# Kernel tuning notes

Measured on AMD Instinct MI355X. Metric: run time of the kernel, lower is better.

## Reference

```python
import jax, jax.numpy as jnp
import numpy as np

SP = 4      # sp_size (number of simulated sequence-parallel ranks)
NH = 16     # num_attention_heads
HD = 64     # head_dim
HS = 1024   # hidden_size
B = 1       # batch
S = 8192    # global sequence length (SP chunks of 2048)


def setup_inputs() -> dict:
    key = jax.random.key(0)
    ks = jax.random.split(key, 9)
    w_scale = 1.0 / np.sqrt(HS)
    def w(k):
        # xavier-ish init, stored as [in, out] so y = x @ W + b
        return jax.random.uniform(k, (HS, HS), jnp.float32, -w_scale, w_scale)
    return {
        'hidden_states': jax.random.normal(ks[0], (B, S, HS), jnp.float32),
        'Wq': w(ks[1]), 'bq': jnp.zeros((HS,), jnp.float32),
        'Wk': w(ks[2]), 'bk': jnp.zeros((HS,), jnp.float32),
        'Wv': w(ks[3]), 'bv': jnp.zeros((HS,), jnp.float32),
        'Wo': w(ks[4]), 'bo': jnp.zeros((HS,), jnp.float32),
    }


def reference(hidden_states, Wq, bq, Wk, bk, Wv, bv, Wo, bo):
    b, s, _ = hidden_states.shape
    sc = s // SP  # per-rank chunk length
    inv_sqrt_hd = 1.0 / np.sqrt(HD)

    def heads(x):
        # [B, S, HS] -> [SP, B, NH, Sc, HD]
        return x.reshape(b, SP, sc, NH, HD).transpose(1, 0, 3, 2, 4)

    q = heads(hidden_states @ Wq + bq)
    k = heads(hidden_states @ Wk + bk)
    v = heads(hidden_states @ Wv + bv)

    out = jnp.zeros_like(q)
    # ring attention: at step i each rank r attends to chunk (r + i) mod SP
    for i in range(SP):
        ki = jnp.roll(k, -i, axis=0)
        vi = jnp.roll(v, -i, axis=0)
        scores = jnp.einsum('sbhqd,sbhkd->sbhqk', q, ki) * inv_sqrt_hd
        probs = jax.nn.softmax(scores, axis=-1)  # per-chunk softmax (faithful to source)
        out = out + jnp.einsum('sbhqk,sbhkd->sbhqd', probs, vi)
    out = out / SP  # source divides accumulated context by sp_size

    # [SP, B, NH, Sc, HD] -> [B, S, NH*HD]
    ctx = out.transpose(1, 0, 3, 2, 4).reshape(b, s, NH * HD)
    return ctx @ Wo + bo
```

## Files before the change

### kernel.cpp

```cpp
#include <hip/hip_runtime.h>

#define DEVINL __device__ __forceinline__

typedef __attribute__((ext_vector_type(8))) short short8;
typedef __attribute__((ext_vector_type(4))) float floatx4;
typedef __attribute__((ext_vector_type(2))) unsigned uintx2;
typedef __attribute__((ext_vector_type(8))) _Float16 halfx8;

DEVINL unsigned short f2bf(float f){
  unsigned u = __builtin_bit_cast(unsigned, f);
  u += 0x7FFFu + ((u >> 16) & 1u);
  return (unsigned short)(u >> 16);
}
DEVINL unsigned pk2(float a, float b){
  unsigned ua = __builtin_bit_cast(unsigned, a);
  unsigned ub = __builtin_bit_cast(unsigned, b);
  ua += 0x7FFFu + ((ua >> 16) & 1u);
  ub += 0x7FFFu + ((ub >> 16) & 1u);
  return (ua >> 16) | (ub & 0xFFFF0000u);
}
DEVINL unsigned pkfast(float a, float b){
  unsigned ua = __builtin_bit_cast(unsigned, a) + 0x8000u;
  unsigned ub = __builtin_bit_cast(unsigned, b) + 0x8000u;
  return __builtin_amdgcn_perm(ub, ua, 0x07060302u);
}
DEVINL float bf2f(unsigned short h){
  unsigned u = ((unsigned)h) << 16;
  return __builtin_bit_cast(float, u);
}
DEVINL void gload_lds16(const void* g, void* l){
  __builtin_amdgcn_global_load_lds((const __attribute__((address_space(1))) void*)g,
                                   (__attribute__((address_space(3))) void*)l, 16, 0, 0);
}
DEVINL int perm2(int k){
  return (((k >> 4) & 1) << 5) | (((k >> 2) & 3) << 3) | (((k >> 5) & 1) << 2) | (k & 3);
}

__global__ void k_detect(const unsigned* __restrict__ w, int* __restrict__ flag){
  __shared__ int cnt;
  if (threadIdx.x == 0) cnt = 0;
  __syncthreads();
  int c = 0;
  for (int i = threadIdx.x; i < 1024; i += 256){
    unsigned e = (w[i] >> 7) & 0xFFu;
    c += (e >= 120u && e <= 132u) ? 1 : 0;
  }
  atomicAdd(&cnt, c);
  __syncthreads();
  if (threadIdx.x == 0) *flag = (cnt > 512) ? 1 : 0;
}

__global__ void k_conv_bf16(const void* __restrict__ src, unsigned short* __restrict__ dst,
                            int n, const int* __restrict__ flag){
  int i = (blockIdx.x * 256 + threadIdx.x) * 8;
  if (i >= n) return;
  if (*flag){
    ((uint4*)dst)[i >> 3] = ((const uint4*)src)[i >> 3];
  } else {
    const float* s = (const float*)src;
    short8 v;
    #pragma unroll
    for (int j = 0; j < 8; j++) v[j] = (short)f2bf(s[i + j]);
    *(short8*)(dst + i) = v;
  }
}

__global__ void k_conv_wT4(const void* __restrict__ s0, const void* __restrict__ s1,
                           const void* __restrict__ s2, const void* __restrict__ s3,
                           unsigned short* __restrict__ d0, unsigned short* __restrict__ d1,
                           unsigned short* __restrict__ d2, unsigned short* __restrict__ d3,
                           const int* __restrict__ flag){
  __shared__ float tile[32][33];
  const void* src; unsigned short* dst;
  switch (blockIdx.z){
    case 0: src = s0; dst = d0; break;
    case 1: src = s1; dst = d1; break;
    case 2: src = s2; dst = d2; break;
    default: src = s3; dst = d3; break;
  }
  const int tx = threadIdx.x & 31, ty = threadIdx.x >> 5;
  const int bx = blockIdx.x, by = blockIdx.y;
  const int isbf = *flag;
  #pragma unroll
  for (int r = 0; r < 32; r += 8){
    int k = by*32 + ty + r, n = bx*32 + tx;
    float v = isbf ? bf2f(((const unsigned short*)src)[k*1024 + n])
                   : ((const float*)src)[k*1024 + n];
    tile[ty + r][tx] = v;
  }
  __syncthreads();
  #pragma unroll
  for (int r = 0; r < 32; r += 8){
    int n = bx*32 + ty + r, k = by*32 + tx;
    dst[n*1024 + k] = f2bf(tile[tx][ty + r]);
  }
}

__global__ void k_conv_b4(const void* __restrict__ s0, const void* __restrict__ s1,
                          const void* __restrict__ s2, const void* __restrict__ s3,
                          float* __restrict__ dst, const int* __restrict__ flag){
  int i = blockIdx.x * 256 + threadIdx.x;
  if (i >= 4096) return;
  int z = i >> 10, j = i & 1023;
  const void* s = (z == 0) ? s0 : (z == 1) ? s1 : (z == 2) ? s2 : s3;
  dst[i] = (*flag) ? bf2f(((const unsigned short*)s)[j]) : ((const float*)s)[j];
}

template<int MODE>
__global__ __launch_bounds__(256, 2) void k_gemm(
    const unsigned short* __restrict__ A, const unsigned short* __restrict__ Bt,
    const float* __restrict__ bias, void* __restrict__ C0, void* __restrict__ C1,
    void* __restrict__ C2, const int* __restrict__ flagp, float scale)
{
  const int K = 1024;
  __shared__ __align__(16) unsigned short As[128*32];
  __shared__ __align__(16) unsigned short Bs[128*32];
  const int tid = threadIdx.x;
  const int lane = tid & 63, wave = tid >> 6;
  const int quad = lane >> 4, l15 = lane & 15;
  const int m0 = blockIdx.x * 128, n0 = blockIdx.y * 128;
  const int wm = (wave >> 1) * 64, wn = (wave & 1) * 64;
  const floatx4 fzero = {0.f, 0.f, 0.f, 0.f};
  floatx4 acc[4][4];
  #pragma unroll
  for (int i = 0; i < 4; i++)
    #pragma unroll
    for (int j = 0; j < 4; j++) acc[i][j] = fzero;

  for (int k0 = 0; k0 < K; k0 += 32){
    __syncthreads();
    #pragma unroll
    for (int rep = 0; rep < 2; rep++){
      int idx = tid + rep*256;
      int row = idx >> 2, c = idx & 3;
      gload_lds16(A  + (size_t)(m0 + row)*K + (k0 + c*8), &As[idx*8]);
      gload_lds16(Bt + (size_t)(n0 + row)*K + (k0 + c*8), &Bs[idx*8]);
    }
    asm volatile("s_waitcnt vmcnt(0)" ::: "memory");
    __syncthreads();
    short8 af[4], bf[4];
    #pragma unroll
    for (int i = 0; i < 4; i++) af[i] = *(const short8*)&As[(wm + i*16 + l15)*32 + quad*8];
    #pragma unroll
    for (int j = 0; j < 4; j++) bf[j] = *(const short8*)&Bs[(wn + j*16 + l15)*32 + quad*8];
    #pragma unroll
    for (int i = 0; i < 4; i++)
      #pragma unroll
      for (int j = 0; j < 4; j++)
        acc[i][j] = __builtin_amdgcn_mfma_f32_16x16x32_bf16(af[i], bf[j], acc[i][j], 0, 0, 0);
  }

  float bs[4];
  #pragma unroll
  for (int j = 0; j < 4; j++) bs[j] = bias[n0 + wn + j*16 + l15];
  const int useBf = (MODE == 1) ? *flagp : 1;
  #pragma unroll
  for (int i = 0; i < 4; i++){
    #pragma unroll
    for (int j = 0; j < 4; j++){
      int n = n0 + wn + j*16 + l15;
      #pragma unroll
      for (int r = 0; r < 4; r++){
        int m = m0 + wm + i*16 + quad*4 + r;
        float v = acc[i][j][r] + bs[j];
        if (MODE == 3){
          int sel = n >> 10, nn = n & 1023;
          if (sel == 0){
            int dd = (nn & 63) ^ ((m & 7) << 3);
            ((unsigned short*)C0)[((size_t)(nn >> 6)*8192 + m)*64 + dd] = f2bf(v * scale);
          } else if (sel == 1){
            int dd = (nn & 63) ^ ((m & 7) << 3);
            ((unsigned short*)C1)[((size_t)(nn >> 6)*8192 + m)*64 + dd] = f2bf(v);
          } else {
            int s2 = perm2(m & 63) ^ ((nn & 7) << 3);
            ((unsigned short*)C2)[(size_t)nn*8192 + (m & ~63) + s2] = f2bf(v);
          }
        } else {
          if (useBf) ((unsigned short*)C0)[(size_t)m*1024 + n] = f2bf(v);
          else       ((float*)C0)[(size_t)m*1024 + n] = v;
        }
      }
    }
  }
}

__global__ __launch_bounds__(256, 4) void k_attn2(
    const unsigned short* __restrict__ Qg, const unsigned short* __restrict__ Kg,
    const unsigned short* __restrict__ Vg, _Float16* __restrict__ part)
{
  __shared__ __align__(16) unsigned short Ks[2][64*64];
  __shared__ __align__(16) unsigned short Vs[2][64*64];
  const int tid = threadIdx.x, lane = tid & 63, wave = tid >> 6;
  const int quad = lane >> 4, l15 = lane & 15;
  const int bid = blockIdx.x;
  const int xcd = bid & 7, slot = bid >> 3;
  const int h = xcd*2 + (slot >> 8);
  const int rem = slot & 255;
  const int c = rem >> 6, qt = rem & 63;
  const int sq0 = qt*128;
  const unsigned short* Qp = Qg + (size_t)h*8192*64 + (size_t)sq0*64;
  const char* Kbase = (const char*)(Kg + (size_t)h*8192*64);
  const char* Vbase = (const char*)(Vg + (size_t)h*8192*64);
  const int wq0 = wave * 32;
  const floatx4 fzero = {0.f, 0.f, 0.f, 0.f};

  const int idx0 = tid, idx1 = tid + 256;
  const unsigned voff0 = (unsigned)(idx0 >> 3)*16384u + (unsigned)(idx0 & 7)*16u;
  const unsigned voff1 = (unsigned)(idx1 >> 3)*16384u + (unsigned)(idx1 & 7)*16u;

  auto stage = [&](int buf, int kvs){
    const char* Kt = Kbase + (size_t)kvs*128;
    const char* Vt = Vbase + (size_t)kvs*2;
    char* kd = (char*)Ks[buf];
    char* vd = (char*)Vs[buf];
    gload_lds16(Kt + idx0*16, kd + idx0*16);
    gload_lds16(Kt + idx1*16, kd + idx1*16);
    gload_lds16(Vt + voff0, vd + idx0*16);
    gload_lds16(Vt + voff1, vd + idx1*16);
  };

  short8 qf[2][2];
  #pragma unroll
  for (int mi = 0; mi < 2; mi++)
    #pragma unroll
    for (int ks = 0; ks < 2; ks++){
      int row = wq0 + mi*16 + l15;
      qf[mi][ks] = *(const short8*)&Qp[row*64 + (((ks*4 + quad) ^ (row & 7)))*8];
    }

  stage(0, c*2048);
  asm volatile("s_waitcnt vmcnt(0)" ::: "memory");
  __syncthreads();

  short8 ones;
  #pragma unroll
  for (int j = 0; j < 8; j++) ones[j] = (short)0x3F80;

  floatx4 Oc[2][4], Ol[2];
  #pragma unroll
  for (int mi = 0; mi < 2; mi++){
    Ol[mi] = fzero;
    #pragma unroll
    for (int di = 0; di < 4; di++) Oc[mi][di] = fzero;
  }

  for (int kt = 0; kt < 32; kt++){
    const int cur = kt & 1;
    asm volatile("s_waitcnt vmcnt(0)" ::: "memory");
    __syncthreads();
    if (kt < 31)
      stage(cur ^ 1, c*2048 + (kt + 1)*64);

    short8 pf[2][2];
    {
      floatx4 S0[4], S1[4];
      #pragma unroll
      for (int ni = 0; ni < 4; ni++){ S0[ni] = fzero; S1[ni] = fzero; }
      #pragma unroll
      for (int ks = 0; ks < 2; ks++)
        #pragma unroll
        for (int ni = 0; ni < 4; ni++){
          int krow = ni*16 + l15;
          short8 kf = *(const short8*)&Ks[cur][krow*64 + (((ks*4 + quad) ^ (krow & 7)))*8];
          S0[ni] = __builtin_amdgcn_mfma_f32_16x16x32_bf16(kf, qf[0][ks], S0[ni], 0, 0, 0);
          S1[ni] = __builtin_amdgcn_mfma_f32_16x16x32_bf16(kf, qf[1][ks], S1[ni], 0, 0, 0);
        }
      #pragma unroll
      for (int ni = 0; ni < 4; ni++)
        #pragma unroll
        for (int r = 0; r < 4; r++){
          S0[ni][r] = __builtin_amdgcn_exp2f(S0[ni][r]);
          S1[ni][r] = __builtin_amdgcn_exp2f(S1[ni][r]);
        }
      #pragma unroll
      for (int ks = 0; ks < 2; ks++){
        uintx2 lo, hi;
        union { uintx2 u[2]; short8 s; } cv;
        lo[0] = pkfast(S0[ks  ][0], S0[ks  ][1]);
        lo[1] = pkfast(S0[ks  ][2], S0[ks  ][3]);
        hi[0] = pkfast(S0[2+ks][0], S0[2+ks][1]);
        hi[1] = pkfast(S0[2+ks][2], S0[2+ks][3]);
        cv.u[0] = lo; cv.u[1] = hi;
        pf[0][ks] = cv.s;
        lo[0] = pkfast(S1[ks  ][0], S1[ks  ][1]);
        lo[1] = pkfast(S1[ks  ][2], S1[ks  ][3]);
        hi[0] = pkfast(S1[2+ks][0], S1[2+ks][1]);
        hi[1] = pkfast(S1[2+ks][2], S1[2+ks][3]);
        cv.u[0] = lo; cv.u[1] = hi;
        pf[1][ks] = cv.s;
      }
    }

    #pragma unroll
    for (int ks = 0; ks < 2; ks++){
      #pragma unroll
      for (int di = 0; di < 4; di++){
        int vrow = di*16 + l15;
        short8 vf = *(const short8*)&Vs[cur][vrow*64 + (((ks*4 + quad) ^ (vrow & 7)))*8];
        Oc[0][di] = __builtin_amdgcn_mfma_f32_16x16x32_bf16(vf, pf[0][ks], Oc[0][di], 0, 0, 0);
        Oc[1][di] = __builtin_amdgcn_mfma_f32_16x16x32_bf16(vf, pf[1][ks], Oc[1][di], 0, 0, 0);
      }
      Ol[0] = __builtin_amdgcn_mfma_f32_16x16x32_bf16(ones, pf[0][ks], Ol[0], 0, 0, 0);
      Ol[1] = __builtin_amdgcn_mfma_f32_16x16x32_bf16(ones, pf[1][ks], Ol[1], 0, 0, 0);
    }
  }

  #pragma unroll
  for (int mi = 0; mi < 2; mi++){
    float inv = __builtin_amdgcn_rcpf(Ol[mi][0]);
    int q = sq0 + wq0 + mi*16 + l15;
    _Float16* dst = part + ((size_t)c*8192 + q)*1024 + h*64;
    #pragma unroll
    for (int di = 0; di < 4; di++){
      union { _Float16 hh[4]; uintx2 u; } w;
      #pragma unroll
      for (int r = 0; r < 4; r++) w.hh[r] = (_Float16)(Oc[mi][di][r] * inv);
      *(uintx2*)(dst + di*16 + quad*4) = w.u;
    }
  }
}

__global__ void k_reduce(const _Float16* __restrict__ part, unsigned short* __restrict__ ctx){
  const size_t N = (size_t)8192*1024;
  size_t i = ((size_t)blockIdx.x*256 + threadIdx.x)*8;
  if (i >= N) return;
  halfx8 a = *(const halfx8*)(part + i);
  halfx8 b = *(const halfx8*)(part + N + i);
  halfx8 c = *(const halfx8*)(part + 2*N + i);
  halfx8 d = *(const halfx8*)(part + 3*N + i);
  short8 o;
  #pragma unroll
  for (int j = 0; j < 8; j++){
    float s = ((float)a[j] + (float)b[j]) + ((float)c[j] + (float)d[j]);
    o[j] = (short)f2bf(s * 0.25f);
  }
  *(short8*)&ctx[i] = o;
}

__global__ __launch_bounds__(256, 2) void k_attn(
    const unsigned short* __restrict__ Qg, const unsigned short* __restrict__ Kg,
    const unsigned short* __restrict__ Vg, unsigned short* __restrict__ ctx)
{
  __shared__ __align__(16) unsigned short Qs[256*64];
  __shared__ __align__(16) unsigned short Ks[2][64*64];
  __shared__ __align__(16) unsigned short Vs[2][64*64];
  const int tid = threadIdx.x, lane = tid & 63, wave = tid >> 6;
  const int quad = lane >> 4, l15 = lane & 15;
  const int bid = blockIdx.x;
  const int xcd = bid & 7, slot = bid >> 3;
  const int h = xcd*2 + (slot >> 5);
  const int rem = slot & 31, rchunk = rem >> 3, qt = rem & 7;
  const int sq0 = rchunk*2048 + qt*256;
  const char* Qbase = (const char*)(Qg + (size_t)h*8192*64 + (size_t)sq0*64);
  const char* Kbase = (const char*)(Kg + (size_t)h*8192*64);
  const char* Vbase = (const char*)(Vg + (size_t)h*8192*64);
  const int wq0 = wave * 64;
  const floatx4 fzero = {0.f, 0.f, 0.f, 0.f};

  const int idx0 = tid, idx1 = tid + 256;
  const size_t voff0 = (size_t)(idx0 >> 3)*16384 + (idx0 & 7)*16;
  const size_t voff1 = (size_t)(idx1 >> 3)*16384 + (idx1 & 7)*16;

  auto stage = [&](int buf, int kvs){
    const char* Kt = Kbase + (size_t)kvs*128;
    const char* Vt = Vbase + (size_t)kvs*2;
    char* kd = (char*)Ks[buf];
    char* vd = (char*)Vs[buf];
    gload_lds16(Kt + idx0*16, kd + idx0*16);
    gload_lds16(Kt + idx1*16, kd + idx1*16);
    gload_lds16(Vt + voff0, vd + idx0*16);
    gload_lds16(Vt + voff1, vd + idx1*16);
  };

  #pragma unroll
  for (int rep = 0; rep < 8; rep++){
    int idx = tid + rep*256;
    gload_lds16(Qbase + idx*16, (char*)Qs + idx*16);
  }
  stage(0, rchunk*2048);
  asm volatile("s_waitcnt vmcnt(0)" ::: "memory");
  __syncthreads();

  short8 qf[4][2];
  #pragma unroll
  for (int mi = 0; mi < 4; mi++)
    #pragma unroll
    for (int ks = 0; ks < 2; ks++){
      int row = wq0 + mi*16 + l15;
      qf[mi][ks] = *(const short8*)&Qs[row*64 + (((ks*4 + quad) ^ (row & 7)))*8];
    }

  short8 ones;
  #pragma unroll
  for (int j = 0; j < 8; j++) ones[j] = (short)0x3F80;

  floatx4 Of[4][4];
  #pragma unroll
  for (int mi = 0; mi < 4; mi++)
    #pragma unroll
    for (int di = 0; di < 4; di++) Of[mi][di] = fzero;

  for (int i = 0; i < 4; i++){
    floatx4 Oc[4][4], Ol[4];
    #pragma unroll
    for (int mi = 0; mi < 4; mi++){
      Ol[mi] = fzero;
      #pragma unroll
      for (int di = 0; di < 4; di++) Oc[mi][di] = fzero;
    }

    for (int kt = 0; kt < 32; kt++){
      const int t = i*32 + kt, cur = t & 1;
      asm volatile("s_waitcnt vmcnt(0)" ::: "memory");
      __syncthreads();
      if (t < 127){
        int t1 = t + 1;
        int kvs = ((rchunk + (t1 >> 5)) & 3)*2048 + (t1 & 31)*64;
        stage(cur ^ 1, kvs);
      }

      short8 pf[4][2];
      #pragma unroll
      for (int mi = 0; mi < 4; mi++){
        floatx4 St[4];
        #pragma unroll
        for (int ni = 0; ni < 4; ni++) St[ni] = fzero;
        #pragma unroll
        for (int ks = 0; ks < 2; ks++)
          #pragma unroll
          for (int ni = 0; ni < 4; ni++){
            int krow = ni*16 + l15;
            short8 kf = *(const short8*)&Ks[cur][krow*64 + (((ks*4 + quad) ^ (krow & 7)))*8];
            St[ni] = __builtin_amdgcn_mfma_f32_16x16x32_bf16(kf, qf[mi][ks], St[ni], 0, 0, 0);
          }
        #pragma unroll
        for (int ni = 0; ni < 4; ni++)
          #pragma unroll
          for (int r = 0; r < 4; r++)
            St[ni][r] = __builtin_amdgcn_exp2f(St[ni][r]);
        #pragma unroll
        for (int ks = 0; ks < 2; ks++){
          uintx2 lo, hi;
          lo[0] = pkfast(St[ks  ][0], St[ks  ][1]);
          lo[1] = pkfast(St[ks  ][2], St[ks  ][3]);
          hi[0] = pkfast(St[2+ks][0], St[2+ks][1]);
          hi[1] = pkfast(St[2+ks][2], St[2+ks][3]);
          union { uintx2 u[2]; short8 s; } cv;
          cv.u[0] = lo; cv.u[1] = hi;
          pf[mi][ks] = cv.s;
        }
      }

      #pragma unroll
      for (int ks = 0; ks < 2; ks++){
        #pragma unroll
        for (int di = 0; di < 4; di++){
          int vrow = di*16 + l15;
          short8 vf = *(const short8*)&Vs[cur][vrow*64 + (((ks*4 + quad) ^ (vrow & 7)))*8];
          #pragma unroll
          for (int mi = 0; mi < 4; mi++)
            Oc[mi][di] = __builtin_amdgcn_mfma_f32_16x16x32_bf16(vf, pf[mi][ks], Oc[mi][di], 0, 0, 0);
        }
        #pragma unroll
        for (int mi = 0; mi < 4; mi++)
          Ol[mi] = __builtin_amdgcn_mfma_f32_16x16x32_bf16(ones, pf[mi][ks], Ol[mi], 0, 0, 0);
      }
    }

    #pragma unroll
    for (int mi = 0; mi < 4; mi++){
      float inv = __builtin_amdgcn_rcpf(Ol[mi][0]);
      #pragma unroll
      for (int di = 0; di < 4; di++)
        #pragma unroll
        for (int r = 0; r < 4; r++) Of[mi][di][r] += Oc[mi][di][r] * inv;
    }
  }

  #pragma unroll
  for (int mi = 0; mi < 4; mi++){
    int q = sq0 + wq0 + mi*16 + l15;
    #pragma unroll
    for (int di = 0; di < 4; di++){
      uintx2 w;
      w[0] = pk2(Of[mi][di][0]*0.25f, Of[mi][di][1]*0.25f);
      w[1] = pk2(Of[mi][di][2]*0.25f, Of[mi][di][3]*0.25f);
      *(uintx2*)&ctx[(size_t)q*1024 + h*64 + di*16 + quad*4] = w;
    }
  }
}

extern "C" void kernel_launch(void* const* d_in, const int* in_sizes, int n_in,
                              void* d_out, int out_size, void* d_ws, size_t ws_size,
                              hipStream_t stream)
{
  (void)in_sizes; (void)n_in; (void)out_size;
  char* ws = (char*)d_ws;
  size_t off = 0;
  auto alloc = [&](size_t bytes) -> char* {
    char* p = ws + off;
    off = (off + bytes + 255) & ~(size_t)255;
    return p;
  };
  int* flag            = (int*)alloc(4);
  unsigned short* hsb  = (unsigned short*)alloc((size_t)8192*1024*2);
  unsigned short* wqt  = (unsigned short*)alloc((size_t)1024*1024*2);
  unsigned short* wkt  = (unsigned short*)alloc((size_t)1024*1024*2);
  unsigned short* wvt  = (unsigned short*)alloc((size_t)1024*1024*2);
  unsigned short* wot  = (unsigned short*)alloc((size_t)1024*1024*2);
  float* biasAll       = (float*)alloc(4096*4);
  unsigned short* Qb   = (unsigned short*)alloc((size_t)16*8192*64*2);
  unsigned short* Kb   = (unsigned short*)alloc((size_t)16*8192*64*2);
  unsigned short* Vb   = (unsigned short*)alloc((size_t)16*8192*64*2);
  unsigned short* ctxb = (unsigned short*)alloc((size_t)8192*1024*2);
  _Float16* part       = (_Float16*)alloc((size_t)4*8192*1024*2);
  const bool wide = (off <= ws_size);

  k_detect<<<1, 256, 0, stream>>>((const unsigned*)d_in[0], flag);
  k_conv_bf16<<<4096, 256, 0, stream>>>(d_in[0], hsb, 8192*1024, flag);
  k_conv_wT4<<<dim3(32,32,4), 256, 0, stream>>>(d_in[1], d_in[3], d_in[5], d_in[7],
                                                wqt, wkt, wvt, wot, flag);
  k_conv_b4<<<16, 256, 0, stream>>>(d_in[2], d_in[4], d_in[6], d_in[8], biasAll, flag);

  const float Cs = 0.18033688011112042f;
  k_gemm<3><<<dim3(64, 24), 256, 0, stream>>>(hsb, wqt, biasAll, Qb, Kb, Vb, nullptr, Cs);

  if (wide){
    k_attn2<<<4096, 256, 0, stream>>>(Qb, Kb, Vb, part);
    k_reduce<<<4096, 256, 0, stream>>>(part, ctxb);
  } else {
    k_attn<<<512, 256, 0, stream>>>(Qb, Kb, Vb, ctxb);
  }

  k_gemm<1><<<dim3(64, 8), 256, 0, stream>>>(ctxb, wot, biasAll + 3072, d_out,
                                             nullptr, nullptr, flag, 1.0f);
}
```

Before: 495.9 us.

## Switch PV path to fp16 MFMA and unroll attention loop with precomputed LDS addresses

V is now stored as fp16 by the projection GEMM, and probabilities are packed with cvt_pkrtz into fp16, so the PV and row-sum MFMAs use the f16 variant instead of bf16. This replaces the manual bf16 rounding and packing of probabilities with a single hardware convert instruction. In k_attn2 the K/V buffers are merged into one LDS array, swizzled base addresses are precomputed, and the tile loop is unrolled by two so buffer offsets become constants. fp16 narrows the representable range of V and P values, which could overflow for large activations.

```diff
diff --git a/kernel.cpp b/kernel.cpp
--- a/kernel.cpp
+++ b/kernel.cpp
@@ -23,6 +23,9 @@
   unsigned ua = __builtin_bit_cast(unsigned, a) + 0x8000u;
   unsigned ub = __builtin_bit_cast(unsigned, b) + 0x8000u;
   return __builtin_amdgcn_perm(ub, ua, 0x07060302u);
+}
+DEVINL unsigned pkh(float a, float b){
+  return __builtin_bit_cast(unsigned, __builtin_amdgcn_cvt_pkrtz(a, b));
 }
 DEVINL float bf2f(unsigned short h){
   unsigned u = ((unsigned)h) << 16;
@@ -173,7 +176,8 @@
             ((unsigned short*)C1)[((size_t)(nn >> 6)*8192 + m)*64 + dd] = f2bf(v);
           } else {
             int s2 = perm2(m & 63) ^ ((nn & 7) << 3);
-            ((unsigned short*)C2)[(size_t)nn*8192 + (m & ~63) + s2] = f2bf(v);
+            ((unsigned short*)C2)[(size_t)nn*8192 + (m & ~63) + s2] =
+                __builtin_bit_cast(unsigned short, (_Float16)v);
           }
         } else {
           if (useBf) ((unsigned short*)C0)[(size_t)m*1024 + n] = f2bf(v);
@@ -188,8 +192,7 @@
     const unsigned short* __restrict__ Qg, const unsigned short* __restrict__ Kg,
     const unsigned short* __restrict__ Vg, _Float16* __restrict__ part)
 {
-  __shared__ __align__(16) unsigned short Ks[2][64*64];
-  __shared__ __align__(16) unsigned short Vs[2][64*64];
+  __shared__ __align__(16) unsigned short KV[2*64*64*2];
   const int tid = threadIdx.x, lane = tid & 63, wave = tid >> 6;
   const int quad = lane >> 4, l15 = lane & 15;
   const int bid = blockIdx.x;
@@ -211,8 +214,8 @@
   auto stage = [&](int buf, int kvs){
     const char* Kt = Kbase + (size_t)kvs*128;
     const char* Vt = Vbase + (size_t)kvs*2;
-    char* kd = (char*)Ks[buf];
-    char* vd = (char*)Vs[buf];
+    char* kd = (char*)KV + buf*8192;
+    char* vd = (char*)KV + 16384 + buf*8192;
     gload_lds16(Kt + idx0*16, kd + idx0*16);
     gload_lds16(Kt + idx1*16, kd + idx1*16);
     gload_lds16(Vt + voff0, vd + idx0*16);
@@ -229,12 +232,22 @@
     }
 
   stage(0, c*2048);
+
+  const int swz0 = ((    quad) ^ (l15 & 7)) * 16;
+  const int swz1 = ((4 + quad) ^ (l15 & 7)) * 16;
+  const char* b0 = (const char*)KV + l15*128 + swz0;
+  const char* b1 = (const char*)KV + l15*128 + swz1;
+
   asm volatile("s_waitcnt vmcnt(0)" ::: "memory");
   __syncthreads();
 
-  short8 ones;
-  #pragma unroll
-  for (int j = 0; j < 8; j++) ones[j] = (short)0x3F80;
+  halfx8 ones;
+  {
+    union { unsigned short s[8]; halfx8 h; } u;
+    #pragma unroll
+    for (int j = 0; j < 8; j++) u.s[j] = 0x3C00;
+    ones = u.h;
+  }
 
   floatx4 Oc[2][4], Ol[2];
   #pragma unroll
@@ -244,66 +257,68 @@
     for (int di = 0; di < 4; di++) Oc[mi][di] = fzero;
   }
 
-  for (int kt = 0; kt < 32; kt++){
-    const int cur = kt & 1;
-    asm volatile("s_waitcnt vmcnt(0)" ::: "memory");
-    __syncthreads();
-    if (kt < 31)
-      stage(cur ^ 1, c*2048 + (kt + 1)*64);
-
-    short8 pf[2][2];
-    {
-      floatx4 S0[4], S1[4];
-      #pragma unroll
-      for (int ni = 0; ni < 4; ni++){ S0[ni] = fzero; S1[ni] = fzero; }
-      #pragma unroll
-      for (int ks = 0; ks < 2; ks++)
-        #pragma unroll
-        for (int ni = 0; ni < 4; ni++){
-          int krow = ni*16 + l15;
-          short8 kf = *(const short8*)&Ks[cur][krow*64 + (((ks*4 + quad) ^ (krow & 7)))*8];
-          S0[ni] = __builtin_amdgcn_mfma_f32_16x16x32_bf16(kf, qf[0][ks], S0[ni], 0, 0, 0);
-          S1[ni] = __builtin_amdgcn_mfma_f32_16x16x32_bf16(kf, qf[1][ks], S1[ni], 0, 0, 0);
-        }
-      #pragma unroll
-      for (int ni = 0; ni < 4; ni++)
-        #pragma unroll
-        for (int r = 0; r < 4; r++){
-          S0[ni][r] = __builtin_amdgcn_exp2f(S0[ni][r]);
-          S1[ni][r] = __builtin_amdgcn_exp2f(S1[ni][r]);
-        }
-      #pragma unroll
-      for (int ks = 0; ks < 2; ks++){
-        uintx2 lo, hi;
-        union { uintx2 u[2]; short8 s; } cv;
-        lo[0] = pkfast(S0[ks  ][0], S0[ks  ][1]);
-        lo[1] = pkfast(S0[ks  ][2], S0[ks  ][3]);
-        hi[0] = pkfast(S0[2+ks][0], S0[2+ks][1]);
-        hi[1] = pkfast(S0[2+ks][2], S0[2+ks][3]);
-        cv.u[0] = lo; cv.u[1] = hi;
-        pf[0][ks] = cv.s;
-        lo[0] = pkfast(S1[ks  ][0], S1[ks  ][1]);
-        lo[1] = pkfast(S1[ks  ][2], S1[ks  ][3]);
-        hi[0] = pkfast(S1[2+ks][0], S1[2+ks][1]);
-        hi[1] = pkfast(S1[2+ks][2], S1[2+ks][3]);
-        cv.u[0] = lo; cv.u[1] = hi;
-        pf[1][ks] = cv.s;
-      }
-    }
-
-    #pragma unroll
-    for (int ks = 0; ks < 2; ks++){
-      #pragma unroll
-      for (int di = 0; di < 4; di++){
-        int vrow = di*16 + l15;
-        short8 vf = *(const short8*)&Vs[cur][vrow*64 + (((ks*4 + quad) ^ (vrow & 7)))*8];
-        Oc[0][di] = __builtin_amdgcn_mfma_f32_16x16x32_bf16(vf, pf[0][ks], Oc[0][di], 0, 0, 0);
-        Oc[1][di] = __builtin_amdgcn_mfma_f32_16x16x32_bf16(vf, pf[1][ks], Oc[1][di], 0, 0, 0);
-      }
-      Ol[0] = __builtin_amdgcn_mfma_f32_16x16x32_bf16(ones, pf[0][ks], Ol[0], 0, 0, 0);
-      Ol[1] = __builtin_amdgcn_mfma_f32_16x16x32_bf16(ones, pf[1][ks], Ol[1], 0, 0, 0);
-    }
-  }
+#define ATTN_TILE(CUR, KT)                                                            \
+  {                                                                                   \
+    asm volatile("s_waitcnt vmcnt(0)" ::: "memory");              \
+    __syncthreads();                                           \
+    if ((KT) < 31)                                                                    \
+      stage((CUR) ^ 1, c*2048 + ((KT) + 1)*64);          \
+    halfx8 pf[2][2];                                                                  \
+    {                                                                                 \
+      floatx4 S0[4], S1[4];                                                           \
+      _Pragma("unroll")                                                               \
+      for (int ni = 0; ni < 4; ni++){ S0[ni] = fzero; S1[ni] = fzero; }               \
+      _Pragma("unroll")                                                               \
+      for (int ni = 0; ni < 4; ni++){                                                 \
+        short8 kf0 = *(const short8*)(b0 + (CUR)*8192 + ni*2048);                     \
+        short8 kf1 = *(const short8*)(b1 + (CUR)*8192 + ni*2048);                     \
+        S0[ni] = __builtin_amdgcn_mfma_f32_16x16x32_bf16(kf0, qf[0][0], S0[ni], 0, 0, 0); \
+        S0[ni] = __builtin_amdgcn_mfma_f32_16x16x32_bf16(kf1, qf[0][1], S0[ni], 0, 0, 0); \
+        S1[ni] = __builtin_amdgcn_mfma_f32_16x16x32_bf16(kf0, qf[1][0], S1[ni], 0, 0, 0); \
+        S1[ni] = __builtin_amdgcn_mfma_f32_16x16x32_bf16(kf1, qf[1][1], S1[ni], 0, 0, 0); \
+      }                                                                               \
+      _Pragma("unroll")                                                               \
+      for (int ni = 0; ni < 4; ni++)                                                  \
+        _Pragma("unroll")                                                             \
+        for (int r = 0; r < 4; r++){                                                  \
+          S0[ni][r] = __builtin_amdgcn_exp2f(S0[ni][r]);                              \
+          S1[ni][r] = __builtin_amdgcn_exp2f(S1[ni][r]);                              \
+        }                                                                             \
+      _Pragma("unroll")                                                               \
+      for (int ks = 0; ks < 2; ks++){                                                 \
+        union { unsigned u[4]; halfx8 h; } cv;                                        \
+        cv.u[0] = pkh(S0[ks  ][0], S0[ks  ][1]);                                      \
+        cv.u[1] = pkh(S0[ks  ][2], S0[ks  ][3]);                                      \
+        cv.u[2] = pkh(S0[2+ks][0], S0[2+ks][1]);                                      \
+        cv.u[3] = pkh(S0[2+ks][2], S0[2+ks][3]);                                      \
+        pf[0][ks] = cv.h;                                                             \
+        cv.u[0] = pkh(S1[ks  ][0], S1[ks  ][1]);                                      \
+        cv.u[1] = pkh(S1[ks  ][2], S1[ks  ][3]);                                      \
+        cv.u[2] = pkh(S1[2+ks][0], S1[2+ks][1]);                                      \
+        cv.u[3] = pkh(S1[2+ks][2], S1[2+ks][3]);                                      \
+        pf[1][ks] = cv.h;                                                             \
+      }                                                                               \
+    }                                                                                 \
+    _Pragma("unroll")                                                                 \
+    for (int ks = 0; ks < 2; ks++){                                                   \
+      const char* vb = ks ? b1 : b0;                                                  \
+      _Pragma("unroll")                                                               \
+      for (int di = 0; di < 4; di++){                                                 \
+        halfx8 vf = __builtin_bit_cast(halfx8,                                        \
+            *(const short8*)(vb + (16384 + (CUR)*8192) + di*2048));                   \
+        Oc[0][di] = __builtin_amdgcn_mfma_f32_16x16x32_f16(vf, pf[0][ks], Oc[0][di], 0, 0, 0); \
+        Oc[1][di] = __builtin_amdgcn_mfma_f32_16x16x32_f16(vf, pf[1][ks], Oc[1][di], 0, 0, 0); \
+      }                                                                               \
+      Ol[0] = __builtin_amdgcn_mfma_f32_16x16x32_f16(ones, pf[0][ks], Ol[0], 0, 0, 0); \
+      Ol[1] = __builtin_amdgcn_mfma_f32_16x16x32_f16(ones, pf[1][ks], Ol[1], 0, 0, 0); \
+    }                                                                                 \
+  }
+
+  for (int kt = 0; kt < 32; kt += 2){
+    ATTN_TILE(0, kt)
+    ATTN_TILE(1, kt + 1)
+  }
+#undef ATTN_TILE
 
   #pragma unroll
   for (int mi = 0; mi < 2; mi++){
@@ -390,9 +405,13 @@
       qf[mi][ks] = *(const short8*)&Qs[row*64 + (((ks*4 + quad) ^ (row & 7)))*8];
     }
 
-  short8 ones;
-  #pragma unroll
-  for (int j = 0; j < 8; j++) ones[j] = (short)0x3F80;
+  halfx8 ones;
+  {
+    union { unsigned short s[8]; halfx8 h; } u;
+    #pragma unroll
+    for (int j = 0; j < 8; j++) u.s[j] = 0x3C00;
+    ones = u.h;
+  }
 
   floatx4 Of[4][4];
   #pragma unroll
@@ -419,7 +438,7 @@
         stage(cur ^ 1, kvs);
       }
 
-      short8 pf[4][2];
+      halfx8 pf[4][2];
       #pragma unroll
       for (int mi = 0; mi < 4; mi++){
         floatx4 St[4];
@@ -440,14 +459,12 @@
             St[ni][r] = __builtin_amdgcn_exp2f(St[ni][r]);
         #pragma unroll
         for (int ks = 0; ks < 2; ks++){
-          uintx2 lo, hi;
-          lo[0] = pkfast(St[ks  ][0], St[ks  ][1]);
-          lo[1] = pkfast(St[ks  ][2], St[ks  ][3]);
-          hi[0] = pkfast(St[2+ks][0], St[2+ks][1]);
-          hi[1] = pkfast(St[2+ks][2], St[2+ks][3]);
-          union { uintx2 u[2]; short8 s; } cv;
-          cv.u[0] = lo; cv.u[1] = hi;
-          pf[mi][ks] = cv.s;
+          union { unsigned u[4]; halfx8 h; } cv;
+          cv.u[0] = pkh(St[ks  ][0], St[ks  ][1]);
+          cv.u[1] = pkh(St[ks  ][2], St[ks  ][3]);
+          cv.u[2] = pkh(St[2+ks][0], St[2+ks][1]);
+          cv.u[3] = pkh(St[2+ks][2], St[2+ks][3]);
+          pf[mi][ks] = cv.h;
         }
       }
 
@@ -456,14 +473,15 @@
         #pragma unroll
         for (int di = 0; di < 4; di++){
           int vrow = di*16 + l15;
-          short8 vf = *(const short8*)&Vs[cur][vrow*64 + (((ks*4 + quad) ^ (vrow & 7)))*8];
+          halfx8 vf = __builtin_bit_cast(halfx8,
+              *(const short8*)&Vs[cur][vrow*64 + (((ks*4 + quad) ^ (vrow & 7)))*8]);
           #pragma unroll
           for (int mi = 0; mi < 4; mi++)
-            Oc[mi][di] = __builtin_amdgcn_mfma_f32_16x16x32_bf16(vf, pf[mi][ks], Oc[mi][di], 0, 0, 0);
+            Oc[mi][di] = __builtin_amdgcn_mfma_f32_16x16x32_f16(vf, pf[mi][ks], Oc[mi][di], 0, 0, 0);
         }
         #pragma unroll
         for (int mi = 0; mi < 4; mi++)
-          Ol[mi] = __builtin_amdgcn_mfma_f32_16x16x32_bf16(ones, pf[mi][ks], Ol[mi], 0, 0, 0);
+          Ol[mi] = __builtin_amdgcn_mfma_f32_16x16x32_f16(ones, pf[mi][ks], Ol[mi], 0, 0, 0);
       }
     }
 
```

New measurement: 500.3 us. About the same (+0.9%).
